# Optimization experiments

Measured on AMD Instinct MI355X. Metric: run time of the kernel, lower is better.

The kernel has to match this reference:

```python
import jax, jax.numpy as jnp
import numpy as np

ROUTING_ITERATIONS = 3


def squash(x):
    # squared norm over the capsule output dim
    sq = jnp.sum(x * x, axis=-1, keepdims=True)
    scale = sq / (1.0 + sq)
    return scale * x / jnp.sqrt(sq)


def setup_inputs() -> dict:
    key = jax.random.key(0)
    k1, k2 = jax.random.split(key)
    B, N, IN_C, K, OUT_C = 256, 1152, 8, 10, 16
    u = jax.random.normal(k1, (B, N, IN_C), dtype=jnp.float32)
    W = jax.random.normal(k2, (K, N, IN_C, OUT_C), dtype=jnp.float32)
    return {"u": u, "W": W}


def reference(u, W):
    # u: [B, N, in_c]; W: [K, N, in_c, out_c]
    # torch: u_hat = matmul(u[None,:,:,None,:], W[:,None]) -> [K, B, N, 1, out_c]
    u_hat = jnp.einsum('bni,knio->kbno', u, W)  # [K, B, N, out_c]
    b_ij = jnp.zeros_like(u_hat)
    v_j = None
    for it in range(ROUTING_ITERATIONS):
        c_ij = jax.nn.softmax(b_ij, axis=2)               # softmax over N, per out_c channel
        s_j = jnp.sum(c_ij * u_hat, axis=2, keepdims=True)  # [K, B, 1, out_c]
        v_j = squash(s_j)
        if it < ROUTING_ITERATIONS - 1:
            a_ij = jnp.sum(u_hat * v_j, axis=-1, keepdims=True)  # [K, B, N, 1]
            b_ij = b_ij + a_ij
    # match torch output shape [K, B, 1, 1, out_c]
    return v_j[:, :, :, None, :]
```

## Files before the change

### kernel.cpp

```cpp
#include <hip/hip_runtime.h>
#include <hip/hip_fp16.h>

#define Bsz 256
#define Nn  1152
#define Kk  10
#define NT  384
#define NW  6
#define S4  1156
#define PAIRS 576

#define W_ELEMS (Kk*Nn*128)
#define U_ELEMS (Bsz*Nn*8)

typedef _Float16 hf2_t __attribute__((ext_vector_type(2)));

static __device__ __forceinline__ unsigned pkh2(float x, float y) {
    __half2 h = __floats2half2_rn(x, y);
    return *reinterpret_cast<unsigned*>(&h);
}
static __device__ __forceinline__ float fdot2u(unsigned a, unsigned b, float c) {
    union { unsigned u; hf2_t h; } A, B;
    A.u = a; B.u = b;
    return __builtin_amdgcn_fdot2(A.h, B.h, c, false);
}
static __device__ __forceinline__ void wave_lds_fence() {
    __builtin_amdgcn_sched_barrier(0);
    asm volatile("s_waitcnt lgkmcnt(0)" ::: "memory");
    __builtin_amdgcn_sched_barrier(0);
}

#define PERM_LO 0x01000504u
#define PERM_HI 0x03020706u
#define ONE2    0x3C003C00u

__global__ void cvt_kernel(const float* __restrict__ W, const float* __restrict__ u,
                           __half2* __restrict__ Wh, __half2* __restrict__ uh) {
    const int idx = blockIdx.x * blockDim.x + threadIdx.x;
    const int wg = W_ELEMS / 8;
    const float4* p;
    __half2* o;
    if (idx < wg) {
        p = (const float4*)W + (size_t)idx * 2;
        o = Wh + (size_t)idx * 4;
    } else {
        const int j = idx - wg;
        p = (const float4*)u + (size_t)j * 2;
        o = uh + (size_t)j * 4;
    }
    const float4 a = p[0], b = p[1];
    o[0] = __floats2half2_rn(a.x, a.y);
    o[1] = __floats2half2_rn(a.z, a.w);
    o[2] = __floats2half2_rn(b.x, b.y);
    o[3] = __floats2half2_rn(b.z, b.w);
}

template<bool HALF>
__global__ __launch_bounds__(NT, 6)
void digitcaps_kernel(const float* __restrict__ u32, const float* __restrict__ W32,
                      const __half* __restrict__ uh, const __half* __restrict__ Wh,
                      float* __restrict__ out)
{
    const int t    = threadIdx.x;
    const int lane = t & 63;
    const int wav  = t >> 6;
    const int b    = blockIdx.x;
    const int k    = blockIdx.y;

    __shared__ unsigned uhS[8 * S4];
    __shared__ unsigned cS2[PAIRS];
    __shared__ float    redS[2][NW][20];

    {
        const int oh = lane & 1;
        const int pr = lane >> 1;
        for (int rr = 0; rr < 6; ++rr) {
            const int n = 192 * rr + 32 * wav + pr;
            float a0[8];
            #pragma unroll
            for (int o = 0; o < 8; ++o) a0[o] = 0.f;
            if (HALF) {
                const uint4 uq = *(const uint4*)(uh + ((size_t)b * Nn + n) * 8);
                const unsigned uw[4] = {uq.x, uq.y, uq.z, uq.w};
                const __half* wbase = Wh + ((size_t)(k * Nn + n)) * 128 + oh * 8;
                #pragma unroll
                for (int p = 0; p < 4; ++p) {
                    const uint4 qa = *(const uint4*)(wbase + (2 * p    ) * 16);
                    const uint4 qb = *(const uint4*)(wbase + (2 * p + 1) * 16);
                    const unsigned aw[4] = {qa.x, qa.y, qa.z, qa.w};
                    const unsigned bw[4] = {qb.x, qb.y, qb.z, qb.w};
                    #pragma unroll
                    for (int jj = 0; jj < 4; ++jj) {
                        const unsigned wl  = __builtin_amdgcn_perm(aw[jj], bw[jj], PERM_LO);
                        const unsigned wh2 = __builtin_amdgcn_perm(aw[jj], bw[jj], PERM_HI);
                        a0[2*jj]   = fdot2u(wl,  uw[p], a0[2*jj]);
                        a0[2*jj+1] = fdot2u(wh2, uw[p], a0[2*jj+1]);
                    }
                }
            } else {
                float ua[8];
                const float4* up = (const float4*)(u32 + ((size_t)b * Nn + n) * 8);
                const float4 x0 = up[0], x1 = up[1];
                ua[0]=x0.x; ua[1]=x0.y; ua[2]=x0.z; ua[3]=x0.w;
                ua[4]=x1.x; ua[5]=x1.y; ua[6]=x1.z; ua[7]=x1.w;
                #pragma unroll
                for (int i = 0; i < 8; ++i) {
                    const float4* wp = (const float4*)(W32 + ((size_t)k * Nn + n) * 128) + oh * 2 + i * 4;
                    const float4 w0 = wp[0], w1 = wp[1];
                    float wv[8];
                    wv[0]=w0.x; wv[1]=w0.y; wv[2]=w0.z; wv[3]=w0.w;
                    wv[4]=w1.x; wv[5]=w1.y; wv[6]=w1.z; wv[7]=w1.w;
                    const float x = ua[i];
                    #pragma unroll
                    for (int o = 0; o < 8; ++o) a0[o] += x * wv[o];
                }
            }
            #pragma unroll
            for (int jj = 0; jj < 4; ++jj)
                uhS[(oh * 4 + jj) * S4 + n] = pkh2(a0[2*jj], a0[2*jj+1]);
        }
    }
    wave_lds_fence();

    float lg[3] = {0.f, 0.f, 0.f};
    unsigned vh[8];
    const int j_s = lane & 7;
    const int g_s = lane >> 3;
    const int l5  = lane >> 5;
    const int l31 = lane & 31;

    #pragma unroll
    for (int it = 0; it < 3; ++it) {
        float m_w = 0.f;
        if (it > 0) {
            #pragma unroll
            for (int j = 0; j < 3; ++j) {
                const int n = 384 * j + 192 * l5 + 32 * wav + l31;
                float acc = 0.f;
                #pragma unroll
                for (int jj = 0; jj < 8; ++jj)
                    acc = fdot2u(uhS[jj * S4 + n], vh[jj], acc);
                lg[j] += acc;
            }
            float m = fmaxf(fmaxf(lg[0], lg[1]), lg[2]);
            #pragma unroll
            for (int off = 1; off <= 32; off <<= 1)
                m = fmaxf(m, __shfl_xor(m, off));
            m_w = m;
            #pragma unroll
            for (int j = 0; j < 3; ++j) {
                const int n = 384 * j + 192 * l5 + 32 * wav + l31;
                const __half eh = __float2half(__expf(lg[j] - m_w));
                ((__half*)cS2)[n] = eh;
            }
            wave_lds_fence();
        }

        float2 sp = {0.f, 0.f};
        float dp = 0.f;
        #pragma unroll
        for (int cc = 0; cc < 12; ++cc) {
            const int P  = g_s + 8 * cc;
            const int n0 = 192 * (P >> 4) + 32 * wav + 2 * (P & 15);
            const unsigned cp = (it == 0) ? ONE2 : cS2[n0 >> 1];
            const uint2 q = *(const uint2*)&uhS[j_s * S4 + n0];
            const unsigned px = __builtin_amdgcn_perm(q.x, q.y, PERM_LO);
            const unsigned py = __builtin_amdgcn_perm(q.x, q.y, PERM_HI);
            sp.x = fdot2u(px, cp, sp.x);
            sp.y = fdot2u(py, cp, sp.y);
            dp   = fdot2u(cp, ONE2, dp);
        }
        #pragma unroll
        for (int off = 8; off <= 32; off <<= 1) {
            sp.x += __shfl_xor(sp.x, off);
            sp.y += __shfl_xor(sp.y, off);
            dp   += __shfl_xor(dp,   off);
        }
        const int buf = it & 1;
        if (lane < 8)
            *(float2*)&redS[buf][wav][2 * j_s] = make_float2(sp.x, sp.y);
        if (lane == 0)
            *(float2*)&redS[buf][wav][16] = make_float2(dp, m_w);
        __syncthreads();

        if (it < 2 || wav == 0) {
            const int o = lane & 15;
            float M = redS[buf][0][17];
            #pragma unroll
            for (int w = 1; w < NW; ++w) M = fmaxf(M, redS[buf][w][17]);
            float s = 0.f, d = 0.f;
            #pragma unroll
            for (int w = 0; w < NW; ++w) {
                const float2 dm = *(const float2*)&redS[buf][w][16];
                const float sc = (it == 0) ? 1.f : __expf(dm.y - M);
                s += sc * redS[buf][w][o];
                d += sc * dm.x;
            }
            s /= d;
            float s2 = s * s;
            #pragma unroll
            for (int off = 1; off <= 8; off <<= 1) s2 += __shfl_xor(s2, off);
            const float scale = (s2 / (1.f + s2)) * rsqrtf(fmaxf(s2, 1e-30f));
            const float v = s * scale;
            if (it == 2) {
                if (wav == 0 && lane < 16)
                    out[((size_t)k * Bsz + b) * 16 + lane] = v;
            } else {
                #pragma unroll
                for (int j = 0; j < 8; ++j)
                    vh[j] = pkh2(__shfl(v, 2*j), __shfl(v, 2*j + 1));
            }
        }
    }
}

extern "C" void kernel_launch(void* const* d_in, const int* in_sizes, int n_in,
                              void* d_out, int out_size, void* d_ws, size_t ws_size,
                              hipStream_t stream) {
    const float* u = (const float*)d_in[0];
    const float* W = (const float*)d_in[1];
    float* out = (float*)d_out;
    const size_t need = (size_t)(W_ELEMS + U_ELEMS) * sizeof(__half);
    if (ws_size >= need) {
        __half* Wh = (__half*)d_ws;
        __half* uh = (__half*)((char*)d_ws + (size_t)W_ELEMS * sizeof(__half));
        cvt_kernel<<<dim3((W_ELEMS + U_ELEMS) / 8 / 256), dim3(256), 0, stream>>>(
            W, u, (__half2*)Wh, (__half2*)uh);
        digitcaps_kernel<true><<<dim3(256, 10), dim3(NT), 0, stream>>>(
            nullptr, nullptr, uh, Wh, out);
    } else {
        digitcaps_kernel<false><<<dim3(256, 10), dim3(NT), 0, stream>>>(
            u, W, nullptr, nullptr, out);
    }
}
```

Measured before the change: 124.8 us.

## Keep u_hat tile in registers instead of LDS for routing iterations

Each thread now keeps its computed fp16 u_hat values for its six N positions in registers, and the routing loop reads them from there. The LDS staging buffer, the coefficient buffer and the wave-level LDS fences are gone. The logit dot products combine the two half-channel lanes with a shuffle, and the weighted sums are reduced across lanes with more shuffles. This removes LDS traffic and frees about 37KB of LDS per block, which can allow more resident blocks. In exchange it adds register pressure and a larger shuffle reduction tree.

```diff
diff --git a/kernel.cpp b/kernel.cpp
--- a/kernel.cpp
+++ b/kernel.cpp
@@ -6,8 +6,6 @@
 #define Kk  10
 #define NT  384
 #define NW  6
-#define S4  1156
-#define PAIRS 576
 
 #define W_ELEMS (Kk*Nn*128)
 #define U_ELEMS (Bsz*Nn*8)
@@ -22,11 +20,6 @@
     union { unsigned u; hf2_t h; } A, B;
     A.u = a; B.u = b;
     return __builtin_amdgcn_fdot2(A.h, B.h, c, false);
-}
-static __device__ __forceinline__ void wave_lds_fence() {
-    __builtin_amdgcn_sched_barrier(0);
-    asm volatile("s_waitcnt lgkmcnt(0)" ::: "memory");
-    __builtin_amdgcn_sched_barrier(0);
 }
 
 #define PERM_LO 0x01000504u
@@ -63,121 +56,120 @@
     const int t    = threadIdx.x;
     const int lane = t & 63;
     const int wav  = t >> 6;
+    const int oh   = lane & 1;
+    const int pr   = lane >> 1;
     const int b    = blockIdx.x;
     const int k    = blockIdx.y;
 
-    __shared__ unsigned uhS[8 * S4];
-    __shared__ unsigned cS2[PAIRS];
-    __shared__ float    redS[2][NW][20];
-
-    {
-        const int oh = lane & 1;
-        const int pr = lane >> 1;
-        for (int rr = 0; rr < 6; ++rr) {
-            const int n = 192 * rr + 32 * wav + pr;
-            float a0[8];
-            #pragma unroll
-            for (int o = 0; o < 8; ++o) a0[o] = 0.f;
-            if (HALF) {
-                const uint4 uq = *(const uint4*)(uh + ((size_t)b * Nn + n) * 8);
-                const unsigned uw[4] = {uq.x, uq.y, uq.z, uq.w};
-                const __half* wbase = Wh + ((size_t)(k * Nn + n)) * 128 + oh * 8;
-                #pragma unroll
-                for (int p = 0; p < 4; ++p) {
-                    const uint4 qa = *(const uint4*)(wbase + (2 * p    ) * 16);
-                    const uint4 qb = *(const uint4*)(wbase + (2 * p + 1) * 16);
-                    const unsigned aw[4] = {qa.x, qa.y, qa.z, qa.w};
-                    const unsigned bw[4] = {qb.x, qb.y, qb.z, qb.w};
-                    #pragma unroll
-                    for (int jj = 0; jj < 4; ++jj) {
-                        const unsigned wl  = __builtin_amdgcn_perm(aw[jj], bw[jj], PERM_LO);
-                        const unsigned wh2 = __builtin_amdgcn_perm(aw[jj], bw[jj], PERM_HI);
-                        a0[2*jj]   = fdot2u(wl,  uw[p], a0[2*jj]);
-                        a0[2*jj+1] = fdot2u(wh2, uw[p], a0[2*jj+1]);
-                    }
+    __shared__ float redS[2][NW][20];
+
+    unsigned uh_r[6][4];
+
+    #pragma unroll
+    for (int rr = 0; rr < 6; ++rr) {
+        const int n = 192 * rr + 32 * wav + pr;
+        float a0[8];
+        #pragma unroll
+        for (int o = 0; o < 8; ++o) a0[o] = 0.f;
+        if (HALF) {
+            const uint4 uq = *(const uint4*)(uh + ((size_t)b * Nn + n) * 8);
+            const unsigned uw[4] = {uq.x, uq.y, uq.z, uq.w};
+            const __half* wbase = Wh + ((size_t)(k * Nn + n)) * 128 + oh * 8;
+            #pragma unroll
+            for (int p = 0; p < 4; ++p) {
+                const uint4 qa = *(const uint4*)(wbase + (2 * p    ) * 16);
+                const uint4 qb = *(const uint4*)(wbase + (2 * p + 1) * 16);
+                const unsigned aw[4] = {qa.x, qa.y, qa.z, qa.w};
+                const unsigned bw[4] = {qb.x, qb.y, qb.z, qb.w};
+                #pragma unroll
+                for (int jj = 0; jj < 4; ++jj) {
+                    const unsigned wl  = __builtin_amdgcn_perm(aw[jj], bw[jj], PERM_LO);
+                    const unsigned wh2 = __builtin_amdgcn_perm(aw[jj], bw[jj], PERM_HI);
+                    a0[2*jj]   = fdot2u(wl,  uw[p], a0[2*jj]);
+                    a0[2*jj+1] = fdot2u(wh2, uw[p], a0[2*jj+1]);
                 }
-            } else {
-                float ua[8];
-                const float4* up = (const float4*)(u32 + ((size_t)b * Nn + n) * 8);
-                const float4 x0 = up[0], x1 = up[1];
-                ua[0]=x0.x; ua[1]=x0.y; ua[2]=x0.z; ua[3]=x0.w;
-                ua[4]=x1.x; ua[5]=x1.y; ua[6]=x1.z; ua[7]=x1.w;
-                #pragma unroll
-                for (int i = 0; i < 8; ++i) {
-                    const float4* wp = (const float4*)(W32 + ((size_t)k * Nn + n) * 128) + oh * 2 + i * 4;
-                    const float4 w0 = wp[0], w1 = wp[1];
-                    float wv[8];
-                    wv[0]=w0.x; wv[1]=w0.y; wv[2]=w0.z; wv[3]=w0.w;
-                    wv[4]=w1.x; wv[5]=w1.y; wv[6]=w1.z; wv[7]=w1.w;
-                    const float x = ua[i];
-                    #pragma unroll
-                    for (int o = 0; o < 8; ++o) a0[o] += x * wv[o];
-                }
-            }
-            #pragma unroll
-            for (int jj = 0; jj < 4; ++jj)
-                uhS[(oh * 4 + jj) * S4 + n] = pkh2(a0[2*jj], a0[2*jj+1]);
-        }
-    }
-    wave_lds_fence();
-
-    float lg[3] = {0.f, 0.f, 0.f};
+            }
+        } else {
+            float ua[8];
+            const float4* up = (const float4*)(u32 + ((size_t)b * Nn + n) * 8);
+            const float4 x0 = up[0], x1 = up[1];
+            ua[0]=x0.x; ua[1]=x0.y; ua[2]=x0.z; ua[3]=x0.w;
+            ua[4]=x1.x; ua[5]=x1.y; ua[6]=x1.z; ua[7]=x1.w;
+            #pragma unroll
+            for (int i = 0; i < 8; ++i) {
+                const float4* wp = (const float4*)(W32 + ((size_t)k * Nn + n) * 128) + oh * 2 + i * 4;
+                const float4 w0 = wp[0], w1 = wp[1];
+                float wv[8];
+                wv[0]=w0.x; wv[1]=w0.y; wv[2]=w0.z; wv[3]=w0.w;
+                wv[4]=w1.x; wv[5]=w1.y; wv[6]=w1.z; wv[7]=w1.w;
+                const float x = ua[i];
+                #pragma unroll
+                for (int o = 0; o < 8; ++o) a0[o] += x * wv[o];
+            }
+        }
+        #pragma unroll
+        for (int jj = 0; jj < 4; ++jj)
+            uh_r[rr][jj] = pkh2(a0[2*jj], a0[2*jj+1]);
+    }
+
+    float lg[6] = {0.f, 0.f, 0.f, 0.f, 0.f, 0.f};
     unsigned vh[8];
-    const int j_s = lane & 7;
-    const int g_s = lane >> 3;
-    const int l5  = lane >> 5;
-    const int l31 = lane & 31;
 
     #pragma unroll
     for (int it = 0; it < 3; ++it) {
         float m_w = 0.f;
+        float c[6];
         if (it > 0) {
             #pragma unroll
-            for (int j = 0; j < 3; ++j) {
-                const int n = 384 * j + 192 * l5 + 32 * wav + l31;
+            for (int rr = 0; rr < 6; ++rr) {
                 float acc = 0.f;
                 #pragma unroll
-                for (int jj = 0; jj < 8; ++jj)
-                    acc = fdot2u(uhS[jj * S4 + n], vh[jj], acc);
-                lg[j] += acc;
-            }
-            float m = fmaxf(fmaxf(lg[0], lg[1]), lg[2]);
+                for (int jj = 0; jj < 4; ++jj)
+                    acc = fdot2u(uh_r[rr][jj], vh[4 * oh + jj], acc);
+                lg[rr] += acc + __shfl_xor(acc, 1);
+            }
+            float m = lg[0];
+            #pragma unroll
+            for (int rr = 1; rr < 6; ++rr) m = fmaxf(m, lg[rr]);
             #pragma unroll
             for (int off = 1; off <= 32; off <<= 1)
                 m = fmaxf(m, __shfl_xor(m, off));
             m_w = m;
             #pragma unroll
-            for (int j = 0; j < 3; ++j) {
-                const int n = 384 * j + 192 * l5 + 32 * wav + l31;
-                const __half eh = __float2half(__expf(lg[j] - m_w));
-                ((__half*)cS2)[n] = eh;
-            }
-            wave_lds_fence();
-        }
-
-        float2 sp = {0.f, 0.f};
+            for (int rr = 0; rr < 6; ++rr) c[rr] = __expf(lg[rr] - m_w);
+        } else {
+            #pragma unroll
+            for (int rr = 0; rr < 6; ++rr) c[rr] = 1.f;
+        }
+
+        float sp[8] = {0.f, 0.f, 0.f, 0.f, 0.f, 0.f, 0.f, 0.f};
         float dp = 0.f;
         #pragma unroll
-        for (int cc = 0; cc < 12; ++cc) {
-            const int P  = g_s + 8 * cc;
-            const int n0 = 192 * (P >> 4) + 32 * wav + 2 * (P & 15);
-            const unsigned cp = (it == 0) ? ONE2 : cS2[n0 >> 1];
-            const uint2 q = *(const uint2*)&uhS[j_s * S4 + n0];
-            const unsigned px = __builtin_amdgcn_perm(q.x, q.y, PERM_LO);
-            const unsigned py = __builtin_amdgcn_perm(q.x, q.y, PERM_HI);
-            sp.x = fdot2u(px, cp, sp.x);
-            sp.y = fdot2u(py, cp, sp.y);
-            dp   = fdot2u(cp, ONE2, dp);
-        }
-        #pragma unroll
-        for (int off = 8; off <= 32; off <<= 1) {
-            sp.x += __shfl_xor(sp.x, off);
-            sp.y += __shfl_xor(sp.y, off);
-            dp   += __shfl_xor(dp,   off);
+        for (int q = 0; q < 3; ++q) {
+            const unsigned cp = pkh2(c[2*q], c[2*q+1]);
+            dp = fdot2u(cp, ONE2, dp);
+            #pragma unroll
+            for (int jj = 0; jj < 4; ++jj) {
+                const unsigned px = __builtin_amdgcn_perm(uh_r[2*q][jj], uh_r[2*q+1][jj], PERM_LO);
+                const unsigned py = __builtin_amdgcn_perm(uh_r[2*q][jj], uh_r[2*q+1][jj], PERM_HI);
+                sp[2*jj]   = fdot2u(px, cp, sp[2*jj]);
+                sp[2*jj+1] = fdot2u(py, cp, sp[2*jj+1]);
+            }
+        }
+        #pragma unroll
+        for (int off = 2; off <= 32; off <<= 1) {
+            #pragma unroll
+            for (int e = 0; e < 8; ++e) sp[e] += __shfl_xor(sp[e], off);
+            dp += __shfl_xor(dp, off);
         }
         const int buf = it & 1;
-        if (lane < 8)
-            *(float2*)&redS[buf][wav][2 * j_s] = make_float2(sp.x, sp.y);
+        if (lane < 2) {
+            float2* dst = (float2*)&redS[buf][wav][8 * lane];
+            dst[0] = make_float2(sp[0], sp[1]);
+            dst[1] = make_float2(sp[2], sp[3]);
+            dst[2] = make_float2(sp[4], sp[5]);
+            dst[3] = make_float2(sp[6], sp[7]);
+        }
         if (lane == 0)
             *(float2*)&redS[buf][wav][16] = make_float2(dp, m_w);
         __syncthreads();
```

Result: slower. 163.6 us (+31.0%).

## Process two batch rows per block, keeping the second row's u_hat in registers

Applied to the files above, without the earlier changes.

Each block now handles two batch elements for one output capsule, so every W load feeds the dot products of both rows and global W traffic is halved. The second row's u_hat is kept in per-thread registers rather than LDS, with its own routing logits, softmax and reductions done through shuffles. The grid is halved and launch bounds drop from 6 to 4 waves' worth of occupancy to make room for the extra registers. The risks are lower occupancy and more register pressure and shuffle work in the routing loop.

```diff
diff --git a/kernel.cpp b/kernel.cpp
--- a/kernel.cpp
+++ b/kernel.cpp
@@ -7,7 +7,6 @@
 #define NT  384
 #define NW  6
 #define S4  1156
-#define PAIRS 576
 
 #define W_ELEMS (Kk*Nn*128)
 #define U_ELEMS (Bsz*Nn*8)
@@ -55,7 +54,7 @@
 }
 
 template<bool HALF>
-__global__ __launch_bounds__(NT, 6)
+__global__ __launch_bounds__(NT, 4)
 void digitcaps_kernel(const float* __restrict__ u32, const float* __restrict__ W32,
                       const __half* __restrict__ uh, const __half* __restrict__ Wh,
                       float* __restrict__ out)
@@ -63,66 +62,81 @@
     const int t    = threadIdx.x;
     const int lane = t & 63;
     const int wav  = t >> 6;
-    const int b    = blockIdx.x;
+    const int oh   = lane & 1;
+    const int pr   = lane >> 1;
+    const int bg   = blockIdx.x;
     const int k    = blockIdx.y;
+    const int b0   = 2 * bg;
+    const int b1   = 2 * bg + 1;
 
     __shared__ unsigned uhS[8 * S4];
-    __shared__ unsigned cS2[PAIRS];
-    __shared__ float    redS[2][NW][20];
-
-    {
-        const int oh = lane & 1;
-        const int pr = lane >> 1;
-        for (int rr = 0; rr < 6; ++rr) {
-            const int n = 192 * rr + 32 * wav + pr;
-            float a0[8];
-            #pragma unroll
-            for (int o = 0; o < 8; ++o) a0[o] = 0.f;
-            if (HALF) {
-                const uint4 uq = *(const uint4*)(uh + ((size_t)b * Nn + n) * 8);
-                const unsigned uw[4] = {uq.x, uq.y, uq.z, uq.w};
-                const __half* wbase = Wh + ((size_t)(k * Nn + n)) * 128 + oh * 8;
-                #pragma unroll
-                for (int p = 0; p < 4; ++p) {
-                    const uint4 qa = *(const uint4*)(wbase + (2 * p    ) * 16);
-                    const uint4 qb = *(const uint4*)(wbase + (2 * p + 1) * 16);
-                    const unsigned aw[4] = {qa.x, qa.y, qa.z, qa.w};
-                    const unsigned bw[4] = {qb.x, qb.y, qb.z, qb.w};
-                    #pragma unroll
-                    for (int jj = 0; jj < 4; ++jj) {
-                        const unsigned wl  = __builtin_amdgcn_perm(aw[jj], bw[jj], PERM_LO);
-                        const unsigned wh2 = __builtin_amdgcn_perm(aw[jj], bw[jj], PERM_HI);
-                        a0[2*jj]   = fdot2u(wl,  uw[p], a0[2*jj]);
-                        a0[2*jj+1] = fdot2u(wh2, uw[p], a0[2*jj+1]);
-                    }
+    __shared__ unsigned cS2u[Nn / 2];
+    __shared__ float    redS[2][2][NW][20];
+
+    unsigned uh_r[6][4];
+
+    #pragma unroll
+    for (int rr = 0; rr < 6; ++rr) {
+        const int n = 192 * rr + 32 * wav + pr;
+        float a0[8], a1[8];
+        #pragma unroll
+        for (int o = 0; o < 8; ++o) { a0[o] = 0.f; a1[o] = 0.f; }
+        if (HALF) {
+            const uint4 uq0 = *(const uint4*)(uh + ((size_t)b0 * Nn + n) * 8);
+            const uint4 uq1 = *(const uint4*)(uh + ((size_t)b1 * Nn + n) * 8);
+            const unsigned uw0[4] = {uq0.x, uq0.y, uq0.z, uq0.w};
+            const unsigned uw1[4] = {uq1.x, uq1.y, uq1.z, uq1.w};
+            const __half* wbase = Wh + ((size_t)(k * Nn + n)) * 128 + oh * 8;
+            #pragma unroll
+            for (int p = 0; p < 4; ++p) {
+                const uint4 qa = *(const uint4*)(wbase + (2 * p    ) * 16);
+                const uint4 qb = *(const uint4*)(wbase + (2 * p + 1) * 16);
+                const unsigned aw[4] = {qa.x, qa.y, qa.z, qa.w};
+                const unsigned bw[4] = {qb.x, qb.y, qb.z, qb.w};
+                #pragma unroll
+                for (int jj = 0; jj < 4; ++jj) {
+                    const unsigned wl  = __builtin_amdgcn_perm(aw[jj], bw[jj], PERM_LO);
+                    const unsigned wh2 = __builtin_amdgcn_perm(aw[jj], bw[jj], PERM_HI);
+                    a0[2*jj]   = fdot2u(wl,  uw0[p], a0[2*jj]);
+                    a0[2*jj+1] = fdot2u(wh2, uw0[p], a0[2*jj+1]);
+                    a1[2*jj]   = fdot2u(wl,  uw1[p], a1[2*jj]);
+                    a1[2*jj+1] = fdot2u(wh2, uw1[p], a1[2*jj+1]);
                 }
-            } else {
-                float ua[8];
-                const float4* up = (const float4*)(u32 + ((size_t)b * Nn + n) * 8);
-                const float4 x0 = up[0], x1 = up[1];
-                ua[0]=x0.x; ua[1]=x0.y; ua[2]=x0.z; ua[3]=x0.w;
-                ua[4]=x1.x; ua[5]=x1.y; ua[6]=x1.z; ua[7]=x1.w;
-                #pragma unroll
-                for (int i = 0; i < 8; ++i) {
-                    const float4* wp = (const float4*)(W32 + ((size_t)k * Nn + n) * 128) + oh * 2 + i * 4;
-                    const float4 w0 = wp[0], w1 = wp[1];
-                    float wv[8];
-                    wv[0]=w0.x; wv[1]=w0.y; wv[2]=w0.z; wv[3]=w0.w;
-                    wv[4]=w1.x; wv[5]=w1.y; wv[6]=w1.z; wv[7]=w1.w;
-                    const float x = ua[i];
-                    #pragma unroll
-                    for (int o = 0; o < 8; ++o) a0[o] += x * wv[o];
-                }
-            }
-            #pragma unroll
-            for (int jj = 0; jj < 4; ++jj)
-                uhS[(oh * 4 + jj) * S4 + n] = pkh2(a0[2*jj], a0[2*jj+1]);
+            }
+        } else {
+            float ua0[8], ua1[8];
+            const float4* up0 = (const float4*)(u32 + ((size_t)b0 * Nn + n) * 8);
+            const float4* up1 = (const float4*)(u32 + ((size_t)b1 * Nn + n) * 8);
+            const float4 x0 = up0[0], x1 = up0[1];
+            const float4 y0 = up1[0], y1 = up1[1];
+            ua0[0]=x0.x; ua0[1]=x0.y; ua0[2]=x0.z; ua0[3]=x0.w;
+            ua0[4]=x1.x; ua0[5]=x1.y; ua0[6]=x1.z; ua0[7]=x1.w;
+            ua1[0]=y0.x; ua1[1]=y0.y; ua1[2]=y0.z; ua1[3]=y0.w;
+            ua1[4]=y1.x; ua1[5]=y1.y; ua1[6]=y1.z; ua1[7]=y1.w;
+            #pragma unroll
+            for (int i = 0; i < 8; ++i) {
+                const float4* wp = (const float4*)(W32 + ((size_t)k * Nn + n) * 128) + oh * 2 + i * 4;
+                const float4 w0 = wp[0], w1 = wp[1];
+                float wv[8];
+                wv[0]=w0.x; wv[1]=w0.y; wv[2]=w0.z; wv[3]=w0.w;
+                wv[4]=w1.x; wv[5]=w1.y; wv[6]=w1.z; wv[7]=w1.w;
+                const float x = ua0[i], y = ua1[i];
+                #pragma unroll
+                for (int o = 0; o < 8; ++o) { a0[o] += x * wv[o]; a1[o] += y * wv[o]; }
+            }
+        }
+        #pragma unroll
+        for (int jj = 0; jj < 4; ++jj) {
+            uhS[(oh * 4 + jj) * S4 + n] = pkh2(a0[2*jj], a0[2*jj+1]);
+            uh_r[rr][jj] = pkh2(a1[2*jj], a1[2*jj+1]);
         }
     }
     wave_lds_fence();
 
-    float lg[3] = {0.f, 0.f, 0.f};
-    unsigned vh[8];
+    float lg0[3] = {0.f, 0.f, 0.f};
+    float lg1[6] = {0.f, 0.f, 0.f, 0.f, 0.f, 0.f};
+    unsigned vh0[8];
+    unsigned vo1[4];
     const int j_s = lane & 7;
     const int g_s = lane >> 3;
     const int l5  = lane >> 5;
@@ -130,7 +144,8 @@
 
     #pragma unroll
     for (int it = 0; it < 3; ++it) {
-        float m_w = 0.f;
+        float m0 = 0.f, m1 = 0.f;
+        float c1[6];
         if (it > 0) {
             #pragma unroll
             for (int j = 0; j < 3; ++j) {
@@ -138,61 +153,110 @@
                 float acc = 0.f;
                 #pragma unroll
                 for (int jj = 0; jj < 8; ++jj)
-                    acc = fdot2u(uhS[jj * S4 + n], vh[jj], acc);
-                lg[j] += acc;
-            }
-            float m = fmaxf(fmaxf(lg[0], lg[1]), lg[2]);
-            #pragma unroll
-            for (int off = 1; off <= 32; off <<= 1)
-                m = fmaxf(m, __shfl_xor(m, off));
-            m_w = m;
+                    acc = fdot2u(uhS[jj * S4 + n], vh0[jj], acc);
+                lg0[j] += acc;
+            }
+            #pragma unroll
+            for (int rr = 0; rr < 6; ++rr) {
+                float acc = 0.f;
+                #pragma unroll
+                for (int jj = 0; jj < 4; ++jj)
+                    acc = fdot2u(uh_r[rr][jj], vo1[jj], acc);
+                lg1[rr] += acc + __shfl_xor(acc, 1);
+            }
+            m0 = fmaxf(fmaxf(lg0[0], lg0[1]), lg0[2]);
+            m1 = fmaxf(fmaxf(fmaxf(lg1[0], lg1[1]), fmaxf(lg1[2], lg1[3])),
+                       fmaxf(lg1[4], lg1[5]));
+            #pragma unroll
+            for (int off = 1; off <= 32; off <<= 1) {
+                m0 = fmaxf(m0, __shfl_xor(m0, off));
+                m1 = fmaxf(m1, __shfl_xor(m1, off));
+            }
             #pragma unroll
             for (int j = 0; j < 3; ++j) {
                 const int n = 384 * j + 192 * l5 + 32 * wav + l31;
-                const __half eh = __float2half(__expf(lg[j] - m_w));
-                ((__half*)cS2)[n] = eh;
-            }
+                ((__half*)cS2u)[n] = __float2half(__expf(lg0[j] - m0));
+            }
+            #pragma unroll
+            for (int rr = 0; rr < 6; ++rr) c1[rr] = __expf(lg1[rr] - m1);
             wave_lds_fence();
-        }
-
-        float2 sp = {0.f, 0.f};
-        float dp = 0.f;
+        } else {
+            #pragma unroll
+            for (int rr = 0; rr < 6; ++rr) c1[rr] = 1.f;
+        }
+
+        float2 sp0 = {0.f, 0.f};
+        float dp0 = 0.f;
         #pragma unroll
         for (int cc = 0; cc < 12; ++cc) {
             const int P  = g_s + 8 * cc;
             const int n0 = 192 * (P >> 4) + 32 * wav + 2 * (P & 15);
-            const unsigned cp = (it == 0) ? ONE2 : cS2[n0 >> 1];
+            const unsigned cp = (it == 0) ? ONE2 : cS2u[n0 >> 1];
             const uint2 q = *(const uint2*)&uhS[j_s * S4 + n0];
             const unsigned px = __builtin_amdgcn_perm(q.x, q.y, PERM_LO);
             const unsigned py = __builtin_amdgcn_perm(q.x, q.y, PERM_HI);
-            sp.x = fdot2u(px, cp, sp.x);
-            sp.y = fdot2u(py, cp, sp.y);
-            dp   = fdot2u(cp, ONE2, dp);
+            sp0.x = fdot2u(px, cp, sp0.x);
+            sp0.y = fdot2u(py, cp, sp0.y);
+            dp0   = fdot2u(cp, ONE2, dp0);
         }
         #pragma unroll
         for (int off = 8; off <= 32; off <<= 1) {
-            sp.x += __shfl_xor(sp.x, off);
-            sp.y += __shfl_xor(sp.y, off);
-            dp   += __shfl_xor(dp,   off);
-        }
+            sp0.x += __shfl_xor(sp0.x, off);
+            sp0.y += __shfl_xor(sp0.y, off);
+            dp0   += __shfl_xor(dp0,   off);
+        }
+
+        float sp1[8] = {0.f, 0.f, 0.f, 0.f, 0.f, 0.f, 0.f, 0.f};
+        float dp1 = 0.f;
+        #pragma unroll
+        for (int q2 = 0; q2 < 3; ++q2) {
+            const unsigned cp1 = pkh2(c1[2*q2], c1[2*q2+1]);
+            dp1 = fdot2u(cp1, ONE2, dp1);
+            #pragma unroll
+            for (int jj = 0; jj < 4; ++jj) {
+                const unsigned px = __builtin_amdgcn_perm(uh_r[2*q2][jj], uh_r[2*q2+1][jj], PERM_LO);
+                const unsigned py = __builtin_amdgcn_perm(uh_r[2*q2][jj], uh_r[2*q2+1][jj], PERM_HI);
+                sp1[2*jj]   = fdot2u(px, cp1, sp1[2*jj]);
+                sp1[2*jj+1] = fdot2u(py, cp1, sp1[2*jj+1]);
+            }
+        }
+        #pragma unroll
+        for (int off = 2; off <= 32; off <<= 1) {
+            #pragma unroll
+            for (int e = 0; e < 8; ++e) sp1[e] += __shfl_xor(sp1[e], off);
+            dp1 += __shfl_xor(dp1, off);
+        }
+
         const int buf = it & 1;
-        if (lane < 8)
-            *(float2*)&redS[buf][wav][2 * j_s] = make_float2(sp.x, sp.y);
-        if (lane == 0)
-            *(float2*)&redS[buf][wav][16] = make_float2(dp, m_w);
+        if (lane < 8) {
+            redS[buf][0][wav][2 * j_s    ] = sp0.x;
+            redS[buf][0][wav][2 * j_s + 1] = sp0.y;
+        }
+        if (lane < 2) {
+            float2* dst = (float2*)&redS[buf][1][wav][8 * lane];
+            dst[0] = make_float2(sp1[0], sp1[1]);
+            dst[1] = make_float2(sp1[2], sp1[3]);
+            dst[2] = make_float2(sp1[4], sp1[5]);
+            dst[3] = make_float2(sp1[6], sp1[7]);
+        }
+        if (lane == 0) {
+            *(float2*)&redS[buf][0][wav][16] = make_float2(dp0, m0);
+            *(float2*)&redS[buf][1][wav][16] = make_float2(dp1, m1);
+        }
         __syncthreads();
 
         if (it < 2 || wav == 0) {
-            const int o = lane & 15;
-            float M = redS[buf][0][17];
-            #pragma unroll
-            for (int w = 1; w < NW; ++w) M = fmaxf(M, redS[buf][w][17]);
+            const int bsel = (lane >> 4) & 1;
+            const int o    = lane & 15;
+            float M = redS[buf][bsel][0][17];
+            #pragma unroll
+            for (int w = 1; w < NW; ++w) M = fmaxf(M, redS[buf][bsel][w][17]);
             float s = 0.f, d = 0.f;
             #pragma unroll
             for (int w = 0; w < NW; ++w) {
-                const float2 dm = *(const float2*)&redS[buf][w][16];
+                const float2 dm = *(const float2*)&redS[buf][bsel][w][16];
                 const float sc = (it == 0) ? 1.f : __expf(dm.y - M);
-                s += sc * redS[buf][w][o];
+                s += sc * redS[buf][bsel][w][o];
                 d += sc * dm.x;
             }
             s /= d;
@@ -202,12 +266,16 @@
             const float scale = (s2 / (1.f + s2)) * rsqrtf(fmaxf(s2, 1e-30f));
             const float v = s * scale;
             if (it == 2) {
-                if (wav == 0 && lane < 16)
-                    out[((size_t)k * Bsz + b) * 16 + lane] = v;
+                if (wav == 0 && lane < 32)
+                    out[((size_t)k * Bsz + b0 + bsel) * 16 + o] = v;
             } else {
                 #pragma unroll
-                for (int j = 0; j < 8; ++j)
-                    vh[j] = pkh2(__shfl(v, 2*j), __shfl(v, 2*j + 1));
+                for (int jj = 0; jj < 8; ++jj)
+                    vh0[jj] = pkh2(__shfl(v, 2 * jj), __shfl(v, 2 * jj + 1));
+                #pragma unroll
+                for (int jj = 0; jj < 4; ++jj)
+                    vo1[jj] = pkh2(__shfl(v, 16 + 8 * oh + 2 * jj),
+                                   __shfl(v, 16 + 8 * oh + 2 * jj + 1));
             }
         }
     }
@@ -225,10 +293,10 @@
         __half* uh = (__half*)((char*)d_ws + (size_t)W_ELEMS * sizeof(__half));
         cvt_kernel<<<dim3((W_ELEMS + U_ELEMS) / 8 / 256), dim3(256), 0, stream>>>(
             W, u, (__half2*)Wh, (__half2*)uh);
-        digitcaps_kernel<true><<<dim3(256, 10), dim3(NT), 0, stream>>>(
+        digitcaps_kernel<true><<<dim3(128, 10), dim3(NT), 0, stream>>>(
             nullptr, nullptr, uh, Wh, out);
     } else {
-        digitcaps_kernel<false><<<dim3(256, 10), dim3(NT), 0, stream>>>(
+        digitcaps_kernel<false><<<dim3(128, 10), dim3(NT), 0, stream>>>(
             u, W, nullptr, nullptr, out);
     }
 }
```

Measured after the change: 121.4 us. -2.7%, faster.
